# Optimization experiments

Measured on AMD Instinct MI355X. Metric: run time of the kernel, lower is better.

## Reference

```python
import jax, jax.numpy as jnp
import numpy as np

N_NODES = 100000
N_EDGES = 1600000
D = 128
N_CLASS = 10
N_LAYERS = 5
BN_EPS = 1e-5


def setup_inputs() -> dict:
    key = jax.random.key(0)
    ks = jax.random.split(key, 8)
    x = jax.random.normal(ks[0], (N_NODES, D), dtype=jnp.float32)
    edge_index = jax.random.randint(ks[1], (2, N_EDGES), 0, N_NODES, dtype=jnp.int32)
    s = 0.05  # small init scale for numerical stability through 5 layers
    W1 = jax.random.normal(ks[2], (N_LAYERS, D, D), dtype=jnp.float32) * s
    b1 = jnp.zeros((N_LAYERS, D), jnp.float32)
    gamma = jnp.ones((N_LAYERS, D), jnp.float32)
    beta = jnp.zeros((N_LAYERS, D), jnp.float32)
    mean = jnp.zeros((N_LAYERS, D), jnp.float32)
    var = jnp.ones((N_LAYERS, D), jnp.float32)
    W2 = jax.random.normal(ks[3], (N_LAYERS, D, D), dtype=jnp.float32) * s
    b2 = jnp.zeros((N_LAYERS, D), jnp.float32)
    lin1_w = jax.random.normal(ks[4], (D, D), dtype=jnp.float32) * s
    lin1_b = jnp.zeros((D,), jnp.float32)
    lin2_w = jax.random.normal(ks[5], (D, N_CLASS), dtype=jnp.float32) * s
    lin2_b = jnp.zeros((N_CLASS,), jnp.float32)
    return {"x": x, "edge_index": edge_index, "W1": W1, "b1": b1,
            "gamma": gamma, "beta": beta, "mean": mean, "var": var,
            "W2": W2, "b2": b2, "lin1_w": lin1_w, "lin1_b": lin1_b,
            "lin2_w": lin2_w, "lin2_b": lin2_b}


def reference(x, edge_index, W1, b1, gamma, beta, mean, var, W2, b2,
              lin1_w, lin1_b, lin2_w, lin2_b):
    n = x.shape[0]
    src, dst = edge_index[0], edge_index[1]
    h = x
    for l in range(N_LAYERS):
        # GIN aggregation: (1+eps)*h + sum_{j->i} h_j, eps=0 (GINConv default)
        agg = jax.ops.segment_sum(h[src], dst, num_segments=n)
        z = (h + agg) @ W1[l] + b1[l]
        # BatchNorm1d in eval mode (running stats)
        z = (z - mean[l]) * (gamma[l] / jnp.sqrt(var[l] + BN_EPS)) + beta[l]
        z = jax.nn.relu(z)
        h = jax.nn.relu(z @ W2[l] + b2[l])
    h = jax.nn.relu(h @ lin1_w + lin1_b)  # dropout is identity in eval
    h = h @ lin2_w + lin2_b
    return jax.nn.log_softmax(h, axis=1)
```

## Files before the change

kernel.cpp:

```cpp
#include <hip/hip_runtime.h>
#include <hip/hip_bf16.h>

#define DD 128

typedef __attribute__((ext_vector_type(8))) short short8;
typedef __attribute__((ext_vector_type(4))) float f32x4;

__device__ __forceinline__ float bf2f(short s) {
    union { unsigned u; float f; } c; c.u = ((unsigned)(unsigned short)s) << 16; return c.f;
}
__device__ __forceinline__ short f2bf(float f) {
    union { float f; unsigned u; } c; c.f = f;
    unsigned u = c.u + 0x7fffu + ((c.u >> 16) & 1u);
    return (short)(u >> 16);
}

__global__ __launch_bounds__(256) void f2b_k(
    const float* __restrict__ x, ushort* __restrict__ o, int n8)
{
    int i = blockIdx.x * 256 + threadIdx.x;
    if (i < n8) {
        float4 v0 = ((const float4*)x)[(size_t)i * 2];
        float4 v1 = ((const float4*)x)[(size_t)i * 2 + 1];
        short8 r;
        r[0] = f2bf(v0.x); r[1] = f2bf(v0.y); r[2] = f2bf(v0.z); r[3] = f2bf(v0.w);
        r[4] = f2bf(v1.x); r[5] = f2bf(v1.y); r[6] = f2bf(v1.z); r[7] = f2bf(v1.w);
        ((short8*)o)[i] = r;
    }
}

__global__ __launch_bounds__(256) void wconv_k(
    const float* __restrict__ W1, const float* __restrict__ W2,
    const float* __restrict__ L1, ushort* __restrict__ Wt)
{
    int idx = blockIdx.x * 256 + threadIdx.x;
    int mat = idx >> 14;
    if (mat >= 11) return;
    int e = idx & 16383;
    int k = e >> 7, n = e & 127;
    const float* src = (mat < 5) ? (W1 + (size_t)mat * 16384)
                     : (mat < 10) ? (W2 + (size_t)(mat - 5) * 16384) : L1;
    float v = src[e];
    int di = (n * 128 + k) ^ ((n & 7) << 3);
    Wt[(size_t)mat * 16384 + di] = (ushort)f2bf(v);
}

__global__ __launch_bounds__(256) void lin2conv_k(
    const float* __restrict__ w, ushort* __restrict__ L2t)
{
    int idx = blockIdx.x * 256 + threadIdx.x;
    if (idx >= 2048) return;
    int c = idx >> 7, k = idx & 127;
    float v = (c < 10) ? w[k * 10 + c] : 0.f;
    L2t[idx] = (ushort)f2bf(v);
}

__global__ __launch_bounds__(256) void hist_k(
    const int* __restrict__ dst, int* __restrict__ cnt, int nEdges)
{
    int e0 = (blockIdx.x * 256 + threadIdx.x) * 4;
    if (e0 + 3 < nEdges) {
        int4 d = *(const int4*)(dst + e0);
        atomicAdd(&cnt[d.x], 1); atomicAdd(&cnt[d.y], 1);
        atomicAdd(&cnt[d.z], 1); atomicAdd(&cnt[d.w], 1);
    } else {
        for (int e = e0; e < nEdges; ++e) atomicAdd(&cnt[dst[e]], 1);
    }
}

__global__ __launch_bounds__(256) void reduce_k(
    const int* __restrict__ cnt, int* __restrict__ bsum, int n)
{
    __shared__ int s[256];
    int t = threadIdx.x;
    int base = blockIdx.x * 1024 + t * 4;
    int v = 0;
    if (base + 3 < n) { int4 c = *(const int4*)(cnt + base); v = c.x + c.y + c.z + c.w; }
    else { for (int i = 0; i < 4; ++i) if (base + i < n) v += cnt[base + i]; }
    s[t] = v; __syncthreads();
    for (int off = 128; off >= 1; off >>= 1) {
        if (t < off) s[t] += s[t + off];
        __syncthreads();
    }
    if (t == 0) bsum[blockIdx.x] = s[0];
}

__global__ __launch_bounds__(128) void scantop_k(
    int* __restrict__ bsum, int* __restrict__ totalOut, int nb)
{
    __shared__ int s[128];
    int t = threadIdx.x;
    int v = (t < nb) ? bsum[t] : 0;
    s[t] = v; __syncthreads();
    for (int off = 1; off < 128; off <<= 1) {
        int u = (t >= off) ? s[t - off] : 0;
        __syncthreads();
        s[t] += u;
        __syncthreads();
    }
    if (t < nb) bsum[t] = s[t] - v;
    if (t == 127) totalOut[0] = s[127];
}

__global__ __launch_bounds__(256) void scanapply_k(
    const int* __restrict__ cnt, const int* __restrict__ bsum,
    int* __restrict__ rowptr, int* __restrict__ cursor, int n)
{
    __shared__ int s[256];
    int t = threadIdx.x;
    int base = blockIdx.x * 1024 + t * 4;
    int c[4]; int v = 0;
    for (int i = 0; i < 4; ++i) { c[i] = (base + i < n) ? cnt[base + i] : 0; v += c[i]; }
    s[t] = v; __syncthreads();
    int mine = v;
    for (int off = 1; off < 256; off <<= 1) {
        int u = (t >= off) ? s[t - off] : 0;
        __syncthreads();
        s[t] += u;
        __syncthreads();
    }
    int run = bsum[blockIdx.x] + s[t] - mine;
    for (int i = 0; i < 4; ++i) {
        if (base + i < n) { rowptr[base + i] = run; cursor[base + i] = run; run += c[i]; }
    }
}

#define FILL_SUB 256
__global__ __launch_bounds__(256) void fill_k(
    const int* __restrict__ src, const int* __restrict__ dst,
    int* __restrict__ cursor, int* __restrict__ csr, int nEdges, int n)
{
    const int r    = blockIdx.x & 7;
    const int sub  = blockIdx.x >> 3;
    const int step = (n + 7) / 8;
    const int rlo  = r * step;
    const int rhi  = min(n, rlo + step);

    for (int base = sub * 1024; base < nEdges; base += FILL_SUB * 1024) {
        int e0 = base + threadIdx.x * 4;
        if (e0 + 3 < nEdges) {
            int4 d = *(const int4*)(dst + e0);
            int4 s = *(const int4*)(src + e0);
            if (d.x >= rlo && d.x < rhi) csr[atomicAdd(&cursor[d.x], 1)] = s.x;
            if (d.y >= rlo && d.y < rhi) csr[atomicAdd(&cursor[d.y], 1)] = s.y;
            if (d.z >= rlo && d.z < rhi) csr[atomicAdd(&cursor[d.z], 1)] = s.z;
            if (d.w >= rlo && d.w < rhi) csr[atomicAdd(&cursor[d.w], 1)] = s.w;
        } else {
            for (int e = e0; e < nEdges; ++e) {
                int d = dst[e];
                if (d >= rlo && d < rhi) csr[atomicAdd(&cursor[d], 1)] = src[e];
            }
        }
    }
}

__global__ __launch_bounds__(256) void gather_bf_k(
    const ushort* __restrict__ h, const int* __restrict__ rowptr,
    const int* __restrict__ csr, ushort* __restrict__ out, int n)
{
    int node = blockIdx.x * 16 + (threadIdx.x >> 4);
    int j = threadIdx.x & 15;
    if (node >= n) return;
    int beg = rowptr[node], end = rowptr[node + 1];
    const short8* hp = (const short8*)h;

    float a[8];
    short8 v = hp[(size_t)node * 16 + j];
#pragma unroll
    for (int i = 0; i < 8; ++i) a[i] = bf2f(v[i]);

    int k = beg;
    for (; k + 3 < end; k += 4) {
        int s0 = csr[k], s1 = csr[k + 1], s2 = csr[k + 2], s3 = csr[k + 3];
        short8 v0 = hp[(size_t)s0 * 16 + j];
        short8 v1 = hp[(size_t)s1 * 16 + j];
        short8 v2 = hp[(size_t)s2 * 16 + j];
        short8 v3 = hp[(size_t)s3 * 16 + j];
#pragma unroll
        for (int i = 0; i < 8; ++i)
            a[i] += (bf2f(v0[i]) + bf2f(v1[i])) + (bf2f(v2[i]) + bf2f(v3[i]));
    }
    for (; k < end; ++k) {
        int s0 = csr[k];
        short8 v0 = hp[(size_t)s0 * 16 + j];
#pragma unroll
        for (int i = 0; i < 8; ++i) a[i] += bf2f(v0[i]);
    }
    short8 r;
#pragma unroll
    for (int i = 0; i < 8; ++i) r[i] = f2bf(a[i]);
    ((short8*)out)[(size_t)node * 16 + j] = r;
}

template <bool BN, int MODE>
__global__ __launch_bounds__(256, 2) void layer_k(
    const ushort* __restrict__ A, const ushort* __restrict__ W1t,
    const float* __restrict__ bias1,
    const float* __restrict__ gamma, const float* __restrict__ beta,
    const float* __restrict__ mean, const float* __restrict__ var,
    const ushort* __restrict__ W2t, const float* __restrict__ bias2,
    ushort* __restrict__ O, float* __restrict__ OUT, int nrows)
{
    __shared__ ushort sA[16384];
    __shared__ ushort sW[16384];
    const int tid  = threadIdx.x;
    const int row0 = blockIdx.x * 128;

    const int lane = tid & 63;
    const int wv   = tid >> 6;
    const int m0   = wv * 32;
    const int lr   = lane & 15;
    const int lg   = lane >> 4;

    short8 w2s[8];
    short8 b2f[4];
    if (MODE == 1) {
#pragma unroll
        for (int i = 0; i < 8; ++i)
            w2s[i] = ((const short8*)W2t)[i * 256 + tid];
    } else {
#pragma unroll
        for (int kk = 0; kk < 4; ++kk)
            b2f[kk] = *(const short8*)(W2t + lr * 128 + kk * 32 + lg * 8);
    }

    {
        const short8* srcv = (const short8*)W1t;
        short8* dstv = (short8*)sW;
#pragma unroll
        for (int i = 0; i < 8; ++i) dstv[i * 256 + tid] = srcv[i * 256 + tid];
    }
#pragma unroll
    for (int i = 0; i < 8; ++i) {
        int f  = i * 256 + tid;
        int r  = f >> 4;
        int c8 = f & 15;
        int gr = row0 + r;
        short8 v = {0, 0, 0, 0, 0, 0, 0, 0};
        if (gr < nrows) v = *(const short8*)(A + (size_t)gr * DD + c8 * 8);
        int db = (r * 256 + c8 * 16) ^ ((r & 7) << 4);
        *(short8*)((char*)sA + db) = v;
    }
    __syncthreads();

    float mul8[8], add8[8];
#pragma unroll
    for (int cf = 0; cf < 8; ++cf) {
        int n = cf * 16 + lr;
        if (BN) {
            float s = gamma[n] * rsqrtf(var[n] + 1e-5f);
            mul8[cf] = s;
            add8[cf] = (bias1[n] - mean[n]) * s + beta[n];
        } else {
            mul8[cf] = 1.f;
            add8[cf] = bias1[n];
        }
    }

    f32x4 acc[2][8];
#pragma unroll
    for (int rf = 0; rf < 2; ++rf)
#pragma unroll
        for (int cf = 0; cf < 8; ++cf) acc[rf][cf] = (f32x4){0.f, 0.f, 0.f, 0.f};

#pragma unroll
    for (int kk = 0; kk < 4; ++kk) {
        const int kb = kk * 64 + lg * 16;
        int ra0 = m0 + lr;
        int ra1 = m0 + 16 + lr;
        short8 a0 = *(short8*)((char*)sA + ((ra0 * 256 + kb) ^ ((ra0 & 7) << 4)));
        short8 a1 = *(short8*)((char*)sA + ((ra1 * 256 + kb) ^ ((ra1 & 7) << 4)));
        short8 b[8];
#pragma unroll
        for (int cf = 0; cf < 8; ++cf) {
            int rn = cf * 16 + lr;
            b[cf] = *(short8*)((char*)sW + ((rn * 256 + kb) ^ ((rn & 7) << 4)));
        }
#pragma unroll
        for (int cf = 0; cf < 8; ++cf) {
            acc[0][cf] = __builtin_amdgcn_mfma_f32_16x16x32_bf16(a0, b[cf], acc[0][cf], 0, 0, 0);
            acc[1][cf] = __builtin_amdgcn_mfma_f32_16x16x32_bf16(a1, b[cf], acc[1][cf], 0, 0, 0);
        }
    }

#pragma unroll
    for (int rf = 0; rf < 2; ++rf)
#pragma unroll
        for (int cf = 0; cf < 8; ++cf) {
            int n = cf * 16 + lr;
#pragma unroll
            for (int i = 0; i < 4; ++i) {
                int row = m0 + rf * 16 + lg * 4 + i;
                float vv = fmaxf(fmaf(acc[rf][cf][i], mul8[cf], add8[cf]), 0.f);
                int db = (row * 256 + n * 2) ^ ((row & 7) << 4);
                *(ushort*)((char*)sA + db) = (ushort)f2bf(vv);
            }
        }

    if (MODE == 1) {
        __syncthreads();
        {
            short8* dstv = (short8*)sW;
#pragma unroll
            for (int i = 0; i < 8; ++i) dstv[i * 256 + tid] = w2s[i];
        }
        __syncthreads();

        f32x4 acc2[2][8];
#pragma unroll
        for (int rf = 0; rf < 2; ++rf)
#pragma unroll
            for (int cf = 0; cf < 8; ++cf) acc2[rf][cf] = (f32x4){0.f, 0.f, 0.f, 0.f};

#pragma unroll
        for (int kk = 0; kk < 4; ++kk) {
            const int kb = kk * 64 + lg * 16;
            int ra0 = m0 + lr;
            int ra1 = m0 + 16 + lr;
            short8 a0 = *(short8*)((char*)sA + ((ra0 * 256 + kb) ^ ((ra0 & 7) << 4)));
            short8 a1 = *(short8*)((char*)sA + ((ra1 * 256 + kb) ^ ((ra1 & 7) << 4)));
            short8 b[8];
#pragma unroll
            for (int cf = 0; cf < 8; ++cf) {
                int rn = cf * 16 + lr;
                b[cf] = *(short8*)((char*)sW + ((rn * 256 + kb) ^ ((rn & 7) << 4)));
            }
#pragma unroll
            for (int cf = 0; cf < 8; ++cf) {
                acc2[0][cf] = __builtin_amdgcn_mfma_f32_16x16x32_bf16(a0, b[cf], acc2[0][cf], 0, 0, 0);
                acc2[1][cf] = __builtin_amdgcn_mfma_f32_16x16x32_bf16(a1, b[cf], acc2[1][cf], 0, 0, 0);
            }
        }

        float add2[8];
#pragma unroll
        for (int cf = 0; cf < 8; ++cf) add2[cf] = bias2[cf * 16 + lr];
#pragma unroll
        for (int rf = 0; rf < 2; ++rf)
#pragma unroll
            for (int cf = 0; cf < 8; ++cf) {
                int n = cf * 16 + lr;
#pragma unroll
                for (int i = 0; i < 4; ++i) {
                    int m = row0 + m0 + rf * 16 + lg * 4 + i;
                    if (m < nrows) {
                        float vv = fmaxf(acc2[rf][cf][i] + add2[cf], 0.f);
                        O[(size_t)m * DD + n] = (ushort)f2bf(vv);
                    }
                }
            }
    } else {
        f32x4 acc2[2];
        acc2[0] = (f32x4){0.f, 0.f, 0.f, 0.f};
        acc2[1] = (f32x4){0.f, 0.f, 0.f, 0.f};
#pragma unroll
        for (int kk = 0; kk < 4; ++kk) {
            const int kb = kk * 64 + lg * 16;
            int ra0 = m0 + lr;
            int ra1 = m0 + 16 + lr;
            short8 a0 = *(short8*)((char*)sA + ((ra0 * 256 + kb) ^ ((ra0 & 7) << 4)));
            short8 a1 = *(short8*)((char*)sA + ((ra1 * 256 + kb) ^ ((ra1 & 7) << 4)));
            acc2[0] = __builtin_amdgcn_mfma_f32_16x16x32_bf16(a0, b2f[kk], acc2[0], 0, 0, 0);
            acc2[1] = __builtin_amdgcn_mfma_f32_16x16x32_bf16(a1, b2f[kk], acc2[1], 0, 0, 0);
        }
        float bc = (lr < 10) ? bias2[lr] : 0.f;
#pragma unroll
        for (int rf = 0; rf < 2; ++rf) {
#pragma unroll
            for (int i = 0; i < 4; ++i) {
                float p = (lr < 10) ? (acc2[rf][i] + bc) : -__builtin_inff();
                float m = p;
#pragma unroll
                for (int off = 8; off >= 1; off >>= 1)
                    m = fmaxf(m, __shfl_xor(m, off, 64));
                float e = expf(p - m);
#pragma unroll
                for (int off = 8; off >= 1; off >>= 1)
                    e += __shfl_xor(e, off, 64);
                float lse = m + logf(e);
                int grow = row0 + m0 + rf * 16 + lg * 4 + i;
                if (lr < 10 && grow < nrows)
                    OUT[(size_t)grow * 10 + lr] = p - lse;
            }
        }
    }
}


extern "C" void kernel_launch(void* const* d_in, const int* in_sizes, int n_in,
                              void* d_out, int out_size, void* d_ws, size_t ws_size,
                              hipStream_t stream)
{
    const float* x      = (const float*)d_in[0];
    const int*   ei     = (const int*)d_in[1];
    const float* W1     = (const float*)d_in[2];
    const float* b1     = (const float*)d_in[3];
    const float* gamma  = (const float*)d_in[4];
    const float* beta   = (const float*)d_in[5];
    const float* mean   = (const float*)d_in[6];
    const float* var    = (const float*)d_in[7];
    const float* W2     = (const float*)d_in[8];
    const float* b2     = (const float*)d_in[9];
    const float* lin1_w = (const float*)d_in[10];
    const float* lin1_b = (const float*)d_in[11];
    const float* lin2_w = (const float*)d_in[12];
    const float* lin2_b = (const float*)d_in[13];

    const int N = in_sizes[0] / DD;
    const int E = in_sizes[1] / 2;
    const int* srcI = ei;
    const int* dstI = ei + E;

    ushort* hb     = (ushort*)d_ws;
    ushort* gb     = hb + (size_t)N * DD;
    ushort* Wt     = gb + (size_t)N * DD;
    ushort* L2t    = Wt + 11 * 16384;
    int*    rowptr = (int*)(L2t + 2048);
    int*    cnt    = rowptr + (N + 4);
    int*    csr    = cnt + N;
    int*    bsum   = csr + E;

    const int nb       = (N + 1023) / 1024;
    const int gemmGrid = (N + 127) / 128;
    const int quadGrid = ((E + 3) / 4 + 255) / 256;

    f2b_k<<<(N * DD / 8 + 255) / 256, 256, 0, stream>>>(x, hb, N * DD / 8);
    wconv_k<<<704, 256, 0, stream>>>(W1, W2, lin1_w, Wt);
    lin2conv_k<<<8, 256, 0, stream>>>(lin2_w, L2t);

    hipMemsetAsync(cnt, 0, (size_t)N * sizeof(int), stream);
    hist_k<<<quadGrid, 256, 0, stream>>>(dstI, cnt, E);
    reduce_k<<<nb, 256, 0, stream>>>(cnt, bsum, N);
    scantop_k<<<1, 128, 0, stream>>>(bsum, rowptr + N, nb);
    scanapply_k<<<nb, 256, 0, stream>>>(cnt, bsum, rowptr, cnt, N);
    fill_k<<<8 * FILL_SUB, 256, 0, stream>>>(srcI, dstI, cnt, csr, E, N);

    for (int l = 0; l < 5; ++l) {
        gather_bf_k<<<(N + 15) / 16, 256, 0, stream>>>(hb, rowptr, csr, gb, N);
        layer_k<true, 1><<<gemmGrid, 256, 0, stream>>>(
            gb, Wt + (size_t)l * 16384, b1 + (size_t)l * DD,
            gamma + (size_t)l * DD, beta + (size_t)l * DD,
            mean + (size_t)l * DD, var + (size_t)l * DD,
            Wt + (size_t)(5 + l) * 16384, b2 + (size_t)l * DD, hb, nullptr, N);
    }
    layer_k<false, 2><<<gemmGrid, 256, 0, stream>>>(
        hb, Wt + (size_t)10 * 16384, lin1_b,
        nullptr, nullptr, nullptr, nullptr,
        L2t, lin2_b, nullptr, (float*)d_out, N);
}
```

Baseline: 625.6 us.

## Sort gather nodes by degree and range-partition histogram atomics

Adds a counting sort of nodes by in-degree (histogram, scan, permutation) so that each gather wave processes nodes with similar degrees, which reduces divergence and load imbalance in the neighbour-sum loop. The edge histogram is also range-partitioned by destination like the fill kernel, which localises its atomics. In exchange it adds three small kernels and a memset, and the gather gains an indirection through perm with less contiguous output writes. Rows for unsorted nodes are still written to their original index, so results are unchanged.

```diff
diff --git a/kernel.cpp b/kernel.cpp
--- a/kernel.cpp
+++ b/kernel.cpp
@@ -55,16 +55,30 @@
     L2t[idx] = (ushort)f2bf(v);
 }
 
+#define RANGE_SUB 256
 __global__ __launch_bounds__(256) void hist_k(
-    const int* __restrict__ dst, int* __restrict__ cnt, int nEdges)
-{
-    int e0 = (blockIdx.x * 256 + threadIdx.x) * 4;
-    if (e0 + 3 < nEdges) {
-        int4 d = *(const int4*)(dst + e0);
-        atomicAdd(&cnt[d.x], 1); atomicAdd(&cnt[d.y], 1);
-        atomicAdd(&cnt[d.z], 1); atomicAdd(&cnt[d.w], 1);
-    } else {
-        for (int e = e0; e < nEdges; ++e) atomicAdd(&cnt[dst[e]], 1);
+    const int* __restrict__ dst, int* __restrict__ cnt, int nEdges, int n)
+{
+    const int r    = blockIdx.x & 7;
+    const int sub  = blockIdx.x >> 3;
+    const int step = (n + 7) / 8;
+    const int rlo  = r * step;
+    const int rhi  = min(n, rlo + step);
+
+    for (int base = sub * 1024; base < nEdges; base += RANGE_SUB * 1024) {
+        int e0 = base + threadIdx.x * 4;
+        if (e0 + 3 < nEdges) {
+            int4 d = *(const int4*)(dst + e0);
+            if (d.x >= rlo && d.x < rhi) atomicAdd(&cnt[d.x], 1);
+            if (d.y >= rlo && d.y < rhi) atomicAdd(&cnt[d.y], 1);
+            if (d.z >= rlo && d.z < rhi) atomicAdd(&cnt[d.z], 1);
+            if (d.w >= rlo && d.w < rhi) atomicAdd(&cnt[d.w], 1);
+        } else {
+            for (int e = e0; e < nEdges; ++e) {
+                int d = dst[e];
+                if (d >= rlo && d < rhi) atomicAdd(&cnt[d], 1);
+            }
+        }
     }
 }
 
@@ -125,7 +139,6 @@
     }
 }
 
-#define FILL_SUB 256
 __global__ __launch_bounds__(256) void fill_k(
     const int* __restrict__ src, const int* __restrict__ dst,
     int* __restrict__ cursor, int* __restrict__ csr, int nEdges, int n)
@@ -136,7 +149,7 @@
     const int rlo  = r * step;
     const int rhi  = min(n, rlo + step);
 
-    for (int base = sub * 1024; base < nEdges; base += FILL_SUB * 1024) {
+    for (int base = sub * 1024; base < nEdges; base += RANGE_SUB * 1024) {
         int e0 = base + threadIdx.x * 4;
         if (e0 + 3 < nEdges) {
             int4 d = *(const int4*)(dst + e0);
@@ -154,13 +167,53 @@
     }
 }
 
+__global__ __launch_bounds__(256) void dhist_k(
+    const int* __restrict__ cnt, int* __restrict__ dh, int n)
+{
+    __shared__ int l[64];
+    int t = threadIdx.x;
+    if (t < 64) l[t] = 0;
+    __syncthreads();
+    int i = blockIdx.x * 256 + t;
+    if (i < n) atomicAdd(&l[min(cnt[i], 63)], 1);
+    __syncthreads();
+    if (t < 64 && l[t]) atomicAdd(&dh[t], l[t]);
+}
+
+__global__ __launch_bounds__(64) void dscan_k(
+    const int* __restrict__ dh, int* __restrict__ dhc)
+{
+    int t = threadIdx.x;
+    int v = dh[t];
+    int s = v;
+#pragma unroll
+    for (int off = 1; off < 64; off <<= 1) {
+        int u = __shfl_up(s, off, 64);
+        if (t >= off) s += u;
+    }
+    dhc[t] = s - v;
+}
+
+__global__ __launch_bounds__(256) void dperm_k(
+    const int* __restrict__ cnt, int* __restrict__ dhc,
+    int* __restrict__ perm, int n)
+{
+    int i = blockIdx.x * 256 + threadIdx.x;
+    if (i < n) {
+        int b = min(cnt[i], 63);
+        perm[atomicAdd(&dhc[b], 1)] = i;
+    }
+}
+
 __global__ __launch_bounds__(256) void gather_bf_k(
     const ushort* __restrict__ h, const int* __restrict__ rowptr,
-    const int* __restrict__ csr, ushort* __restrict__ out, int n)
-{
-    int node = blockIdx.x * 16 + (threadIdx.x >> 4);
+    const int* __restrict__ csr, const int* __restrict__ perm,
+    ushort* __restrict__ out, int n)
+{
+    int g = blockIdx.x * 16 + (threadIdx.x >> 4);
     int j = threadIdx.x & 15;
-    if (node >= n) return;
+    if (g >= n) return;
+    int node = perm[g];
     int beg = rowptr[node], end = rowptr[node + 1];
     const short8* hp = (const short8*)h;
 
@@ -419,24 +472,31 @@
     int*    cnt    = rowptr + (N + 4);
     int*    csr    = cnt + N;
     int*    bsum   = csr + E;
+    int*    perm   = bsum + 128;
+    int*    dh     = perm + N;
+    int*    dhc    = dh + 64;
 
     const int nb       = (N + 1023) / 1024;
     const int gemmGrid = (N + 127) / 128;
-    const int quadGrid = ((E + 3) / 4 + 255) / 256;
+    const int nodeGrid = (N + 255) / 256;
 
     f2b_k<<<(N * DD / 8 + 255) / 256, 256, 0, stream>>>(x, hb, N * DD / 8);
     wconv_k<<<704, 256, 0, stream>>>(W1, W2, lin1_w, Wt);
     lin2conv_k<<<8, 256, 0, stream>>>(lin2_w, L2t);
 
     hipMemsetAsync(cnt, 0, (size_t)N * sizeof(int), stream);
-    hist_k<<<quadGrid, 256, 0, stream>>>(dstI, cnt, E);
+    hipMemsetAsync(dh, 0, 64 * sizeof(int), stream);
+    hist_k<<<8 * RANGE_SUB, 256, 0, stream>>>(dstI, cnt, E, N);
+    dhist_k<<<nodeGrid, 256, 0, stream>>>(cnt, dh, N);
+    dscan_k<<<1, 64, 0, stream>>>(dh, dhc);
+    dperm_k<<<nodeGrid, 256, 0, stream>>>(cnt, dhc, perm, N);
     reduce_k<<<nb, 256, 0, stream>>>(cnt, bsum, N);
     scantop_k<<<1, 128, 0, stream>>>(bsum, rowptr + N, nb);
     scanapply_k<<<nb, 256, 0, stream>>>(cnt, bsum, rowptr, cnt, N);
-    fill_k<<<8 * FILL_SUB, 256, 0, stream>>>(srcI, dstI, cnt, csr, E, N);
+    fill_k<<<8 * RANGE_SUB, 256, 0, stream>>>(srcI, dstI, cnt, csr, E, N);
 
     for (int l = 0; l < 5; ++l) {
-        gather_bf_k<<<(N + 15) / 16, 256, 0, stream>>>(hb, rowptr, csr, gb, N);
+        gather_bf_k<<<(N + 15) / 16, 256, 0, stream>>>(hb, rowptr, csr, perm, gb, N);
         layer_k<true, 1><<<gemmGrid, 256, 0, stream>>>(
             gb, Wt + (size_t)l * 16384, b1 + (size_t)l * DD,
             gamma + (size_t)l * DD, beta + (size_t)l * DD,
```

New measurement: 944.4 us. 51.0% more time.
